# Kernel optimization log

Hardware: AMD Instinct MI355X
Metric: run time of the kernel (lower is better)

The kernel has to match this reference:

```python
import jax, jax.numpy as jnp
import numpy as np

B, T = 64, 2048
QD, KD, VD, AD = 512, 512, 512, 256


def setup_inputs() -> dict:
    key = jax.random.key(0)
    ks = jax.random.split(key, 9)
    s = lambda d: 1.0 / np.sqrt(d)
    return {
        "query": jax.random.normal(ks[0], (B, QD), jnp.float32),
        "key": jax.random.normal(ks[1], (B, T, KD), jnp.float32),
        "value": jax.random.normal(ks[2], (B, T, VD), jnp.float32),
        "Wq": jax.random.uniform(ks[3], (QD, AD), jnp.float32, -s(QD), s(QD)),
        "bq": jax.random.uniform(ks[4], (AD,), jnp.float32, -s(QD), s(QD)),
        "Wk": jax.random.uniform(ks[5], (KD, AD), jnp.float32, -s(KD), s(KD)),
        "bk": jax.random.uniform(ks[6], (AD,), jnp.float32, -s(KD), s(KD)),
        "Wo": jax.random.uniform(ks[7], (AD, 1), jnp.float32, -s(AD), s(AD)),
        "bo": jax.random.uniform(ks[8], (1,), jnp.float32, -s(AD), s(AD)),
    }


def reference(query, key, value, Wq, bq, Wk, bk, Wo, bo):
    # q_proj: [B, 1, AD]; k_proj: [B, T, AD]
    q_proj = (query @ Wq + bq)[:, None, :]
    k_proj = jnp.einsum("btk,ka->bta", key, Wk) + bk
    # score: [B, T, 1]
    score = jnp.tanh(q_proj + k_proj) @ Wo + bo
    attn = jax.nn.softmax(score, axis=1)  # softmax over keys (dim 1)
    # context: [B, VD] = sum_t attn[b,t] * value[b,t,:]
    context = jnp.einsum("bt,btv->bv", attn[..., 0], value)
    return context, attn[..., 0]
```

## Files before the change

kernel.cpp:

```cpp
#include <hip/hip_runtime.h>

#define NB 64
#define NT 2048
#define NQD 512
#define NKD 512
#define NVD 512
#define NAD 256

typedef __attribute__((ext_vector_type(8))) short s16x8;
typedef __attribute__((ext_vector_type(4))) float fx4;
typedef __attribute__((ext_vector_type(4))) unsigned int u32x4;

__device__ __forceinline__ short f2bf(float x) {
  union { float f; unsigned u; } v; v.f = x;
  return (short)((v.u + 0x7fffu + ((v.u >> 16) & 1u)) >> 16);
}

__device__ __forceinline__ unsigned cvt_pk_bf16(float lo, float hi) {
  unsigned r;
  asm("v_cvt_pk_bf16_f32 %0, %1, %2" : "=v"(r) : "v"(lo), "v"(hi));
  return r;
}

__device__ __forceinline__ float fast_tanh(float x) {
  float e = __expf(x + x);
  return 1.0f - 2.0f * __builtin_amdgcn_rcpf(e + 1.0f);
}

__device__ __forceinline__ void gload_lds16(const void* g, void* l) {
  __builtin_amdgcn_global_load_lds(
      (const __attribute__((address_space(1))) unsigned int*)g,
      (__attribute__((address_space(3))) unsigned int*)l, 16, 0, 0);
}

__global__ void prep_kernel(const float* __restrict__ query, const float* __restrict__ Wq,
                            const float* __restrict__ bq, const float* __restrict__ bk,
                            const float* __restrict__ Wk,
                            float* __restrict__ qpk, short* __restrict__ Bpk) {
  __shared__ float q[NQD];
  const int tid = threadIdx.x;
  if (blockIdx.x < NB) {
    const int b = blockIdx.x;
    for (int k = tid; k < NQD; k += 256) q[k] = query[b * NQD + k];
    __syncthreads();
    float acc = bq[tid] + bk[tid];
#pragma unroll 8
    for (int k = 0; k < NQD; ++k) acc += q[k] * Wq[k * NAD + tid];
    qpk[b * NAD + tid] = acc;
  } else {
    const int ks = blockIdx.x - NB;
#pragma unroll
    for (int rep = 0; rep < 4; ++rep) {
      const int o = rep * 256 + tid;
      const int wnt = o >> 6;
      const int l = o & 63;
      const int g = l >> 4, h = l & 15;
      const int n = wnt * 16 + h;
      const int k0 = ks * 32 + g * 8;
      s16x8 v;
#pragma unroll
      for (int j = 0; j < 8; ++j) v[j] = f2bf(Wk[(size_t)(k0 + j) * NAD + n]);
      *(s16x8*)(Bpk + (size_t)(ks * 1024 + o) * 8) = v;
    }
  }
}

__global__ void __launch_bounds__(256, 3)
score_kernel(const float* __restrict__ key, const short* __restrict__ Bpk,
             const float* __restrict__ qpk, const float* __restrict__ Wo,
             float* __restrict__ score) {
  __shared__ float As[2][64 * 32];
  __shared__ short Bs[2][256 * 32];
  __shared__ float sred[4][64];
  const int tid = threadIdx.x;
  const int w = tid >> 6, l = tid & 63;
  const int g = l >> 4, h = l & 15;
  const int m0 = blockIdx.x * 64;
  const int b = m0 >> 11;

  const float* srcA[2];
  int loffA[2];
#pragma unroll
  for (int i = 0; i < 2; ++i) {
    const int p = w * 128 + i * 64 + l;
    const int row = p >> 3, c = p & 7;
    srcA[i] = key + (size_t)(m0 + row) * NKD + ((c ^ (row & 7)) << 2);
    loffA[i] = (w * 128 + i * 64) * 16;
  }
  const short* srcB[4];
  int loffB[4];
#pragma unroll
  for (int i = 0; i < 4; ++i) {
    const int o = w * 256 + i * 64 + l;
    srcB[i] = Bpk + (size_t)o * 8;
    loffB[i] = (w * 256 + i * 64) * 16;
  }

  auto stageA = [&](int bb, int ck) {
#pragma unroll
    for (int i = 0; i < 2; ++i)
      gload_lds16(srcA[i] + ck * 32, (char*)&As[bb][0] + loffA[i]);
  };
  auto stageB = [&](int bb, int ck) {
#pragma unroll
    for (int i = 0; i < 4; ++i)
      gload_lds16(srcB[i] + (size_t)ck * 8192, (char*)&Bs[bb][0] + loffB[i]);
  };

  stageA(0, 0); stageB(0, 0);
  stageA(1, 1); stageB(1, 1);

  fx4 acc[4][4];
#pragma unroll
  for (int i = 0; i < 4; ++i)
#pragma unroll
    for (int j = 0; j < 4; ++j) acc[i][j] = fx4{0.f, 0.f, 0.f, 0.f};

  for (int ck = 0; ck < 16; ++ck) {
    const int buf = ck & 1;
    if (ck < 15) asm volatile("s_waitcnt vmcnt(6)" ::: "memory");
    else         asm volatile("s_waitcnt vmcnt(0)" ::: "memory");
    __builtin_amdgcn_sched_barrier(0);
    __builtin_amdgcn_s_barrier();

    s16x8 af[4], bfr[4];
#pragma unroll
    for (int mt = 0; mt < 4; ++mt) {
      const int R = mt * 16 + h;
      const char* base = (const char*)&As[buf][0] + R * 128;
      fx4 lo = *(const fx4*)(base + (((g * 2    ) ^ (R & 7)) << 4));
      fx4 hi = *(const fx4*)(base + (((g * 2 + 1) ^ (R & 7)) << 4));
      u32x4 uu;
      uu[0] = cvt_pk_bf16(lo[0], lo[1]);
      uu[1] = cvt_pk_bf16(lo[2], lo[3]);
      uu[2] = cvt_pk_bf16(hi[0], hi[1]);
      uu[3] = cvt_pk_bf16(hi[2], hi[3]);
      af[mt] = *(s16x8*)&uu;
    }
#pragma unroll
    for (int nt = 0; nt < 4; ++nt)
      bfr[nt] = *(const s16x8*)((const char*)&Bs[buf][0] + (w * 256 + nt * 64 + l) * 16);
#pragma unroll
    for (int mt = 0; mt < 4; ++mt)
#pragma unroll
      for (int nt = 0; nt < 4; ++nt)
        acc[mt][nt] = __builtin_amdgcn_mfma_f32_16x16x32_bf16(af[mt], bfr[nt], acc[mt][nt], 0, 0, 0);

    __builtin_amdgcn_s_barrier();
    if (ck < 14) { stageA(buf, ck + 2); stageB(buf, ck + 2); }
  }

  float qv[4], wv[4];
#pragma unroll
  for (int nt = 0; nt < 4; ++nt) {
    const int n = w * 64 + nt * 16 + h;
    qv[nt] = qpk[b * NAD + n];
    wv[nt] = Wo[n];
  }
#pragma unroll
  for (int mt = 0; mt < 4; ++mt) {
#pragma unroll
    for (int rr = 0; rr < 4; ++rr) {
      float s = fast_tanh(acc[mt][0][rr] + qv[0]) * wv[0]
              + fast_tanh(acc[mt][1][rr] + qv[1]) * wv[1]
              + fast_tanh(acc[mt][2][rr] + qv[2]) * wv[2]
              + fast_tanh(acc[mt][3][rr] + qv[3]) * wv[3];
#pragma unroll
      for (int off = 1; off < 16; off <<= 1) s += __shfl_xor(s, off, 64);
      if (h == 0) sred[w][mt * 16 + g * 4 + rr] = s;
    }
  }
  __syncthreads();
  if (tid < 64)
    score[m0 + tid] = sred[0][tid] + sred[1][tid] + sred[2][tid] + sred[3][tid];
}

__global__ void softmax_kernel(const float* __restrict__ score, float* __restrict__ attn) {
  __shared__ float redm[4];
  __shared__ float reds[4];
  const int b = blockIdx.x, tid = threadIdx.x;
  const float* s = score + (size_t)b * NT;
  float v[8];
  float m = -3.0e38f;
#pragma unroll
  for (int j = 0; j < 8; ++j) { v[j] = s[tid + j * 256]; m = fmaxf(m, v[j]); }
#pragma unroll
  for (int off = 1; off < 64; off <<= 1) m = fmaxf(m, __shfl_xor(m, off, 64));
  if ((tid & 63) == 0) redm[tid >> 6] = m;
  __syncthreads();
  m = fmaxf(fmaxf(redm[0], redm[1]), fmaxf(redm[2], redm[3]));
  float sum = 0.f;
#pragma unroll
  for (int j = 0; j < 8; ++j) { v[j] = __expf(v[j] - m); sum += v[j]; }
#pragma unroll
  for (int off = 1; off < 64; off <<= 1) sum += __shfl_xor(sum, off, 64);
  if ((tid & 63) == 0) reds[tid >> 6] = sum;
  __syncthreads();
  sum = reds[0] + reds[1] + reds[2] + reds[3];
  const float inv = 1.0f / sum;
#pragma unroll
  for (int j = 0; j < 8; ++j) attn[(size_t)b * NT + tid + j * 256] = v[j] * inv;
}

__global__ void ctx_partial_kernel(const float* __restrict__ attn, const float* __restrict__ value,
                                   float* __restrict__ partial) {
  __shared__ float a[64];
  __shared__ fx4 red[128];
  const int blk = blockIdx.x;
  const int b = blk >> 5, tc = blk & 31;
  const int tid = threadIdx.x;
  if (tid < 64) a[tid] = attn[(size_t)b * NT + tc * 64 + tid];
  __syncthreads();
  const int half = tid >> 7;
  const int vi = (tid & 127) * 4;
  const float* vp = value + ((size_t)b * NT + tc * 64 + half) * NVD + vi;
  fx4 s = fx4{0.f, 0.f, 0.f, 0.f};
#pragma unroll 8
  for (int t = 0; t < 64; t += 2) {
    fx4 x = *(const fx4*)(vp + (size_t)t * NVD);
    const float wt = a[t + half];
    s += x * wt;
  }
  if (half) red[tid & 127] = s;
  __syncthreads();
  if (!half) {
    s += red[tid];
    *(fx4*)(partial + (size_t)blk * NVD + vi) = s;
  }
}

__global__ void ctx_reduce_kernel(const float* __restrict__ partial, float* __restrict__ ctx) {
  const int i = blockIdx.x * 256 + threadIdx.x;
  const int b = i >> 9, v = i & (NVD - 1);
  float s = 0.f;
#pragma unroll
  for (int tc = 0; tc < 32; ++tc) s += partial[(size_t)(b * 32 + tc) * NVD + v];
  ctx[i] = s;
}

extern "C" void kernel_launch(void* const* d_in, const int* in_sizes, int n_in,
                              void* d_out, int out_size, void* d_ws, size_t ws_size,
                              hipStream_t stream) {
  const float* query = (const float*)d_in[0];
  const float* key   = (const float*)d_in[1];
  const float* value = (const float*)d_in[2];
  const float* Wq    = (const float*)d_in[3];
  const float* bq    = (const float*)d_in[4];
  const float* Wk    = (const float*)d_in[5];
  const float* bk    = (const float*)d_in[6];
  const float* Wo    = (const float*)d_in[7];

  float* out  = (float*)d_out;
  float* ctx  = out;
  float* attn = out + NB * NVD;

  char* ws = (char*)d_ws;
  float* qpk     = (float*)(ws);
  short* Bpk     = (short*)(ws + 64 * 1024);
  float* score   = (float*)(ws + (64 + 256) * 1024);
  float* partial = (float*)(ws + (64 + 256 + 512) * 1024);

  prep_kernel<<<NB + 16, 256, 0, stream>>>(query, Wq, bq, bk, Wk, qpk, Bpk);
  score_kernel<<<(NB * NT) / 64, 256, 0, stream>>>(key, Bpk, qpk, Wo, score);
  softmax_kernel<<<NB, 256, 0, stream>>>(score, attn);
  ctx_partial_kernel<<<NB * 32, 256, 0, stream>>>(attn, value, partial);
  ctx_reduce_kernel<<<(NB * NVD) / 256, 256, 0, stream>>>(partial, ctx);
}
```

Baseline: 167.9 us.

## Double score-kernel M tile to 128 rows with 8 waves sharing Wk tile

The score GEMM block grows from 64 to 128 rows of key and from 4 to 8 waves arranged 2x4, so each staged Wk chunk in LDS is reused across twice as many rows. This halves the per-row B-operand global/LDS traffic, and the loads per thread are rebalanced to 2+2. The A-fragment conversion is also interleaved with the MFMAs to shorten register live ranges. In exchange LDS use per block rises and the grid has half as many blocks, which may reduce occupancy and latency hiding.

```diff
diff --git a/kernel.cpp b/kernel.cpp
--- a/kernel.cpp
+++ b/kernel.cpp
@@ -65,50 +65,49 @@
   }
 }
 
-__global__ void __launch_bounds__(256, 3)
+__global__ void __launch_bounds__(512, 4)
 score_kernel(const float* __restrict__ key, const short* __restrict__ Bpk,
              const float* __restrict__ qpk, const float* __restrict__ Wo,
              float* __restrict__ score) {
-  __shared__ float As[2][64 * 32];
+  __shared__ float As[2][128 * 32];
   __shared__ short Bs[2][256 * 32];
-  __shared__ float sred[4][64];
+  __shared__ float sred[4][128];
   const int tid = threadIdx.x;
-  const int w = tid >> 6, l = tid & 63;
+  const int W = tid >> 6, l = tid & 63;
+  const int wr = W >> 2, wc = W & 3;
   const int g = l >> 4, h = l & 15;
-  const int m0 = blockIdx.x * 64;
+  const int m0 = blockIdx.x * 128;
   const int b = m0 >> 11;
 
   const float* srcA[2];
   int loffA[2];
 #pragma unroll
   for (int i = 0; i < 2; ++i) {
-    const int p = w * 128 + i * 64 + l;
+    const int p = W * 128 + i * 64 + l;
     const int row = p >> 3, c = p & 7;
     srcA[i] = key + (size_t)(m0 + row) * NKD + ((c ^ (row & 7)) << 2);
-    loffA[i] = (w * 128 + i * 64) * 16;
-  }
-  const short* srcB[4];
-  int loffB[4];
-#pragma unroll
-  for (int i = 0; i < 4; ++i) {
-    const int o = w * 256 + i * 64 + l;
+    loffA[i] = (W * 128 + i * 64) * 16;
+  }
+  const short* srcB[2];
+  int loffB[2];
+#pragma unroll
+  for (int i = 0; i < 2; ++i) {
+    const int o = W * 128 + i * 64 + l;
     srcB[i] = Bpk + (size_t)o * 8;
-    loffB[i] = (w * 256 + i * 64) * 16;
-  }
-
-  auto stageA = [&](int bb, int ck) {
+    loffB[i] = (W * 128 + i * 64) * 16;
+  }
+
+  auto stage = [&](int bb, int ck) {
 #pragma unroll
     for (int i = 0; i < 2; ++i)
       gload_lds16(srcA[i] + ck * 32, (char*)&As[bb][0] + loffA[i]);
-  };
-  auto stageB = [&](int bb, int ck) {
-#pragma unroll
-    for (int i = 0; i < 4; ++i)
+#pragma unroll
+    for (int i = 0; i < 2; ++i)
       gload_lds16(srcB[i] + (size_t)ck * 8192, (char*)&Bs[bb][0] + loffB[i]);
   };
 
-  stageA(0, 0); stageB(0, 0);
-  stageA(1, 1); stageB(1, 1);
+  stage(0, 0);
+  stage(1, 1);
 
   fx4 acc[4][4];
 #pragma unroll
@@ -118,15 +117,18 @@
 
   for (int ck = 0; ck < 16; ++ck) {
     const int buf = ck & 1;
-    if (ck < 15) asm volatile("s_waitcnt vmcnt(6)" ::: "memory");
+    if (ck < 15) asm volatile("s_waitcnt vmcnt(4)" ::: "memory");
     else         asm volatile("s_waitcnt vmcnt(0)" ::: "memory");
     __builtin_amdgcn_sched_barrier(0);
     __builtin_amdgcn_s_barrier();
 
-    s16x8 af[4], bfr[4];
+    s16x8 bfr[4];
+#pragma unroll
+    for (int nt = 0; nt < 4; ++nt)
+      bfr[nt] = *(const s16x8*)((const char*)&Bs[buf][0] + ((wc * 4 + nt) * 64 + l) * 16);
 #pragma unroll
     for (int mt = 0; mt < 4; ++mt) {
-      const int R = mt * 16 + h;
+      const int R = wr * 64 + mt * 16 + h;
       const char* base = (const char*)&As[buf][0] + R * 128;
       fx4 lo = *(const fx4*)(base + (((g * 2    ) ^ (R & 7)) << 4));
       fx4 hi = *(const fx4*)(base + (((g * 2 + 1) ^ (R & 7)) << 4));
@@ -135,25 +137,20 @@
       uu[1] = cvt_pk_bf16(lo[2], lo[3]);
       uu[2] = cvt_pk_bf16(hi[0], hi[1]);
       uu[3] = cvt_pk_bf16(hi[2], hi[3]);
-      af[mt] = *(s16x8*)&uu;
+      const s16x8 af = *(s16x8*)&uu;
+#pragma unroll
+      for (int nt = 0; nt < 4; ++nt)
+        acc[mt][nt] = __builtin_amdgcn_mfma_f32_16x16x32_bf16(af, bfr[nt], acc[mt][nt], 0, 0, 0);
     }
-#pragma unroll
-    for (int nt = 0; nt < 4; ++nt)
-      bfr[nt] = *(const s16x8*)((const char*)&Bs[buf][0] + (w * 256 + nt * 64 + l) * 16);
-#pragma unroll
-    for (int mt = 0; mt < 4; ++mt)
-#pragma unroll
-      for (int nt = 0; nt < 4; ++nt)
-        acc[mt][nt] = __builtin_amdgcn_mfma_f32_16x16x32_bf16(af[mt], bfr[nt], acc[mt][nt], 0, 0, 0);
 
     __builtin_amdgcn_s_barrier();
-    if (ck < 14) { stageA(buf, ck + 2); stageB(buf, ck + 2); }
+    if (ck < 14) stage(buf, ck + 2);
   }
 
   float qv[4], wv[4];
 #pragma unroll
   for (int nt = 0; nt < 4; ++nt) {
-    const int n = w * 64 + nt * 16 + h;
+    const int n = wc * 64 + nt * 16 + h;
     qv[nt] = qpk[b * NAD + n];
     wv[nt] = Wo[n];
   }
@@ -167,11 +164,11 @@
               + fast_tanh(acc[mt][3][rr] + qv[3]) * wv[3];
 #pragma unroll
       for (int off = 1; off < 16; off <<= 1) s += __shfl_xor(s, off, 64);
-      if (h == 0) sred[w][mt * 16 + g * 4 + rr] = s;
+      if (h == 0) sred[wc][wr * 64 + mt * 16 + g * 4 + rr] = s;
     }
   }
   __syncthreads();
-  if (tid < 64)
+  if (tid < 128)
     score[m0 + tid] = sred[0][tid] + sred[1][tid] + sred[2][tid] + sred[3][tid];
 }
 
@@ -261,7 +258,7 @@
   float* partial = (float*)(ws + (64 + 256 + 512) * 1024);
 
   prep_kernel<<<NB + 16, 256, 0, stream>>>(query, Wq, bq, bk, Wk, qpk, Bpk);
-  score_kernel<<<(NB * NT) / 64, 256, 0, stream>>>(key, Bpk, qpk, Wo, score);
+  score_kernel<<<(NB * NT) / 128, 512, 0, stream>>>(key, Bpk, qpk, Wo, score);
   softmax_kernel<<<NB, 256, 0, stream>>>(score, attn);
   ctx_partial_kernel<<<NB * 32, 256, 0, stream>>>(attn, value, partial);
   ctx_reduce_kernel<<<(NB * NVD) / 256, 256, 0, stream>>>(partial, ctx);
```

Measured after the change: 152.2 us. 1.1x faster.

## Load full 32-row key tile into LDS and read Wk fragments from global

Applied to the files above, without the earlier changes.

The score kernel now processes 32 rows per block instead of 64. It loads the whole 32x512 fp32 key tile into LDS in one shot with an XOR swizzle, then runs all 16 K-steps without double buffering. The packed bf16 Wk fragments are read straight from global/L2 into registers instead of being staged through LDS. This drops the per-step barriers and the B-side LDS traffic, at the cost of a larger LDS footprint (64KB, lower occupancy), no overlap between load and compute within a block, and twice as many blocks each re-reading Wk.

```diff
diff --git a/kernel.cpp b/kernel.cpp
--- a/kernel.cpp
+++ b/kernel.cpp
@@ -65,71 +65,54 @@
   }
 }
 
-__global__ void __launch_bounds__(256, 3)
+__global__ void __launch_bounds__(256, 2)
 score_kernel(const float* __restrict__ key, const short* __restrict__ Bpk,
              const float* __restrict__ qpk, const float* __restrict__ Wo,
              float* __restrict__ score) {
-  __shared__ float As[2][64 * 32];
-  __shared__ short Bs[2][256 * 32];
-  __shared__ float sred[4][64];
+  __shared__ float As[32 * 512];
+  __shared__ float sred[4][32];
   const int tid = threadIdx.x;
   const int w = tid >> 6, l = tid & 63;
   const int g = l >> 4, h = l & 15;
-  const int m0 = blockIdx.x * 64;
+  const int m0 = blockIdx.x * 32;
   const int b = m0 >> 11;
 
-  const float* srcA[2];
-  int loffA[2];
-#pragma unroll
-  for (int i = 0; i < 2; ++i) {
-    const int p = w * 128 + i * 64 + l;
-    const int row = p >> 3, c = p & 7;
-    srcA[i] = key + (size_t)(m0 + row) * NKD + ((c ^ (row & 7)) << 2);
-    loffA[i] = (w * 128 + i * 64) * 16;
-  }
-  const short* srcB[4];
-  int loffB[4];
-#pragma unroll
-  for (int i = 0; i < 4; ++i) {
-    const int o = w * 256 + i * 64 + l;
-    srcB[i] = Bpk + (size_t)o * 8;
-    loffB[i] = (w * 256 + i * 64) * 16;
-  }
-
-  auto stageA = [&](int bb, int ck) {
-#pragma unroll
-    for (int i = 0; i < 2; ++i)
-      gload_lds16(srcA[i] + ck * 32, (char*)&As[bb][0] + loffA[i]);
-  };
-  auto stageB = [&](int bb, int ck) {
-#pragma unroll
-    for (int i = 0; i < 4; ++i)
-      gload_lds16(srcB[i] + (size_t)ck * 8192, (char*)&Bs[bb][0] + loffB[i]);
-  };
-
-  stageA(0, 0); stageB(0, 0);
-  stageA(1, 1); stageB(1, 1);
-
-  fx4 acc[4][4];
-#pragma unroll
-  for (int i = 0; i < 4; ++i)
+  {
+    const char* tile = (const char*)(key + (size_t)m0 * NKD);
+#pragma unroll
+    for (int i = 0; i < 16; ++i) {
+      const int q = (w * 16 + i) * 64 + l;
+      const int row = q >> 7;
+      const int col = q & 127;
+      const int sg = col ^ (row & 15);
+      gload_lds16(tile + ((size_t)row * 128 + sg) * 16,
+                  (char*)As + (size_t)(w * 16 + i) * 1024);
+    }
+  }
+  __syncthreads();
+
+  const short* bbase = Bpk + (size_t)(w * 256 + l) * 8;
+
+  fx4 acc[2][4];
+#pragma unroll
+  for (int i = 0; i < 2; ++i)
 #pragma unroll
     for (int j = 0; j < 4; ++j) acc[i][j] = fx4{0.f, 0.f, 0.f, 0.f};
 
-  for (int ck = 0; ck < 16; ++ck) {
-    const int buf = ck & 1;
-    if (ck < 15) asm volatile("s_waitcnt vmcnt(6)" ::: "memory");
-    else         asm volatile("s_waitcnt vmcnt(0)" ::: "memory");
-    __builtin_amdgcn_sched_barrier(0);
-    __builtin_amdgcn_s_barrier();
-
-    s16x8 af[4], bfr[4];
-#pragma unroll
-    for (int mt = 0; mt < 4; ++mt) {
+#pragma unroll
+  for (int ks = 0; ks < 16; ++ks) {
+    s16x8 bfr[4];
+#pragma unroll
+    for (int nt = 0; nt < 4; ++nt)
+      bfr[nt] = *(const s16x8*)(bbase + (size_t)ks * 8192 + nt * 512);
+    s16x8 af[2];
+#pragma unroll
+    for (int mt = 0; mt < 2; ++mt) {
       const int R = mt * 16 + h;
-      const char* base = (const char*)&As[buf][0] + R * 128;
-      fx4 lo = *(const fx4*)(base + (((g * 2    ) ^ (R & 7)) << 4));
-      fx4 hi = *(const fx4*)(base + (((g * 2 + 1) ^ (R & 7)) << 4));
+      const int kc = ks * 8 + g * 2;
+      const float* base = As + (size_t)R * 128 * 4;
+      fx4 lo = *(const fx4*)(base + (size_t)(kc ^ h) * 4);
+      fx4 hi = *(const fx4*)(base + (size_t)((kc + 1) ^ h) * 4);
       u32x4 uu;
       uu[0] = cvt_pk_bf16(lo[0], lo[1]);
       uu[1] = cvt_pk_bf16(lo[2], lo[3]);
@@ -138,16 +121,10 @@
       af[mt] = *(s16x8*)&uu;
     }
 #pragma unroll
-    for (int nt = 0; nt < 4; ++nt)
-      bfr[nt] = *(const s16x8*)((const char*)&Bs[buf][0] + (w * 256 + nt * 64 + l) * 16);
-#pragma unroll
-    for (int mt = 0; mt < 4; ++mt)
+    for (int mt = 0; mt < 2; ++mt)
 #pragma unroll
       for (int nt = 0; nt < 4; ++nt)
         acc[mt][nt] = __builtin_amdgcn_mfma_f32_16x16x32_bf16(af[mt], bfr[nt], acc[mt][nt], 0, 0, 0);
-
-    __builtin_amdgcn_s_barrier();
-    if (ck < 14) { stageA(buf, ck + 2); stageB(buf, ck + 2); }
   }
 
   float qv[4], wv[4];
@@ -158,7 +135,7 @@
     wv[nt] = Wo[n];
   }
 #pragma unroll
-  for (int mt = 0; mt < 4; ++mt) {
+  for (int mt = 0; mt < 2; ++mt) {
 #pragma unroll
     for (int rr = 0; rr < 4; ++rr) {
       float s = fast_tanh(acc[mt][0][rr] + qv[0]) * wv[0]
@@ -171,7 +148,7 @@
     }
   }
   __syncthreads();
-  if (tid < 64)
+  if (tid < 32)
     score[m0 + tid] = sred[0][tid] + sred[1][tid] + sred[2][tid] + sred[3][tid];
 }
 
@@ -261,7 +238,7 @@
   float* partial = (float*)(ws + (64 + 256 + 512) * 1024);
 
   prep_kernel<<<NB + 16, 256, 0, stream>>>(query, Wq, bq, bk, Wk, qpk, Bpk);
-  score_kernel<<<(NB * NT) / 64, 256, 0, stream>>>(key, Bpk, qpk, Wo, score);
+  score_kernel<<<(NB * NT) / 32, 256, 0, stream>>>(key, Bpk, qpk, Wo, score);
   softmax_kernel<<<NB, 256, 0, stream>>>(score, attn);
   ctx_partial_kernel<<<NB * 32, 256, 0, stream>>>(attn, value, partial);
   ctx_reduce_kernel<<<(NB * NVD) / 256, 256, 0, stream>>>(partial, ctx);
```

Measured after the change: 192.0 us. +14.4%, slower.
